# Kernel optimization log

Hardware: AMD Instinct MI355X
Metric: run time of the kernel (lower is better)

Reference implementation:

```python
import jax, jax.numpy as jnp
import numpy as np

N, E, F, H, C, G = 100000, 800000, 128, 128, 10, 128
EPS = 1e-5


def setup_inputs() -> dict:
    key = jax.random.key(0)
    ks = jax.random.split(key, 8)
    return {
        "x": jax.random.normal(ks[0], (N, F), jnp.float32),
        "edge_index": jax.random.randint(ks[1], (2, E), 0, N),
        "batch": jnp.sort(jax.random.randint(ks[2], (N,), 0, G)),
        "edge_weight": jax.random.uniform(ks[3], (E,), jnp.float32, 0.1, 1.0),
        "bn_feat_w": jnp.ones((F,), jnp.float32),
        "bn_feat_b": jnp.full((F,), 1e-4, jnp.float32),
        "conv_feat_W": jax.random.normal(ks[4], (F, H), jnp.float32) / np.float32(np.sqrt(F)),
        "conv_feat_b": jnp.zeros((H,), jnp.float32),
        "bns_w": jnp.ones((3, H), jnp.float32),
        "bns_b": jnp.full((3, H), 1e-4, jnp.float32),
        "convs_W": jax.random.normal(ks[5], (3, H, H), jnp.float32) / np.float32(np.sqrt(H)),
        "convs_b": jnp.zeros((3, H), jnp.float32),
        "bn_fc_w": jnp.ones((H,), jnp.float32),
        "bn_fc_b": jnp.full((H,), 1e-4, jnp.float32),
        "lin_fc_W": jax.random.normal(ks[6], (H, H), jnp.float32) / np.float32(np.sqrt(H)),
        "lin_fc_b": jnp.zeros((H,), jnp.float32),
        "bn_hidden_w": jnp.ones((H,), jnp.float32),
        "bn_hidden_b": jnp.full((H,), 1e-4, jnp.float32),
        "lin_class_W": jax.random.normal(ks[7], (H, C), jnp.float32) / np.float32(np.sqrt(H)),
        "lin_class_b": jnp.zeros((C,), jnp.float32),
    }


def _bn(h, w, b):
    # training-mode BatchNorm1d: biased batch stats over dim 0
    mu = h.mean(0)
    var = jnp.mean((h - mu) ** 2, 0)
    return (h - mu) * jax.lax.rsqrt(var + EPS) * w + b


def reference(x, edge_index, batch, edge_weight,
              bn_feat_w, bn_feat_b, conv_feat_W, conv_feat_b,
              bns_w, bns_b, convs_W, convs_b,
              bn_fc_w, bn_fc_b, lin_fc_W, lin_fc_b,
              bn_hidden_w, bn_hidden_b, lin_class_W, lin_class_b):
    n = x.shape[0]
    loops = jnp.arange(n)
    # PyG GCNConv: add self-loops (weight 1) + symmetric normalization, shared by all convs
    row = jnp.concatenate([edge_index[0], loops])
    col = jnp.concatenate([edge_index[1], loops])
    ew = jnp.concatenate([edge_weight, jnp.ones((n,), x.dtype)])
    deg = jax.ops.segment_sum(ew, col, num_segments=n)
    dinv = jnp.where(deg > 0, jax.lax.rsqrt(jnp.maximum(deg, EPS)), 0.0)
    norm = (dinv[row] * ew * dinv[col])[:, None]  # [E+N, 1]

    def conv(h, W, b):
        m = (h @ W)[row] * norm                 # gather + scale per edge
        return jax.ops.segment_sum(m, col, num_segments=n) + b

    h = _bn(x, bn_feat_w, bn_feat_b)
    h = jax.nn.relu(conv(h, conv_feat_W, conv_feat_b))
    h_init = h

    x_list = []
    # branch 1: BN -> Conv -> ReLU chain
    h = h_init
    for i in range(3):
        h = jax.nn.relu(conv(_bn(h, bns_w[i], bns_b[i]), convs_W[i], convs_b[i]))
    x_list.append(h)
    # branch 2: double application of the same BN/Conv per step
    h = h_init
    for i in range(3):
        h_ = jax.nn.relu(conv(_bn(h, bns_w[i], bns_b[i]), convs_W[i], convs_b[i]))
        h = jax.nn.relu(conv(_bn(h_, bns_w[i], bns_b[i]), convs_W[i], convs_b[i]))
    x_list.append(h)
    # branch 3: identical to branch 1 when conv_residual=False
    h = h_init
    for i in range(3):
        h = jax.nn.relu(conv(_bn(h, bns_w[i], bns_b[i]), convs_W[i], convs_b[i]))
    x_list.append(h)
    # branch 4: BN -> ReLU only
    h = h_init
    for i in range(3):
        h = jax.nn.relu(_bn(h, bns_w[i], bns_b[i]))
    x_list.append(h)

    def head(hn):
        g = jax.ops.segment_sum(hn, batch, num_segments=G)  # global_add_pool
        g = jax.nn.relu(_bn(g, bn_fc_w, bn_fc_b) @ lin_fc_W + lin_fc_b)
        g = _bn(g, bn_hidden_w, bn_hidden_b)
        return jax.nn.log_softmax(g @ lin_class_W + lin_class_b, axis=-1)

    return tuple(head(hn) for hn in x_list)
```

## Files before the change

### kernel.cpp

```cpp
#include <hip/hip_runtime.h>

#define N_NODES 100000
#define NPAD    100032
#define NBLK    1563
#define NEDGE   800000
#define NGRP    128
#define NSLOT   32
#define EPS     1e-5f

typedef unsigned int   u32;
typedef unsigned short u16;
typedef short bf16x8 __attribute__((ext_vector_type(8)));
typedef float f32x4  __attribute__((ext_vector_type(4)));

__device__ __forceinline__ float bf2f(u32 u){ return __uint_as_float(u << 16); }
__device__ __forceinline__ u16 f2bf(float f){
  u32 x = __float_as_uint(f);
  x += 0x7fffu + ((x >> 16) & 1u);
  return (u16)(x >> 16);
}

__global__ void k_init(float* deg, int* cnt, int* fill, float* gbuf){
  int i = blockIdx.x * 256 + threadIdx.x;
  if (i < NPAD){ deg[i] = 1.0f; cnt[i] = 0; fill[i] = 0; }
  if (i < 4 * NGRP * 128) gbuf[i] = 0.f;
}

__global__ void k_deg(const int* __restrict__ col, const float* __restrict__ ew,
                      float* __restrict__ deg, int* __restrict__ cnt){
  int e = blockIdx.x * 256 + threadIdx.x;
  if (e < NEDGE){
    int c = col[e];
    atomicAdd(&deg[c], ew[e]);
    atomicAdd(&cnt[c], 1);
  }
}

__global__ void k_dinv(const float* __restrict__ deg, float* __restrict__ dinv, float* __restrict__ srow){
  int i = blockIdx.x * 256 + threadIdx.x;
  if (i < N_NODES){
    float d = deg[i];
    float v = d > 0.f ? rsqrtf(fmaxf(d, EPS)) : 0.f;
    dinv[i] = v; srow[i] = v * v;
  }
}

__global__ __launch_bounds__(256) void k_chunksum(const int* __restrict__ cnt, int* __restrict__ csum){
  int b = blockIdx.x, t = threadIdx.x;
  int s = 0;
  for (int i = t; i < 1024; i += 256){ int idx = b * 1024 + i; if (idx < N_NODES) s += cnt[idx]; }
  __shared__ int red[256];
  red[t] = s; __syncthreads();
  for (int o = 128; o > 0; o >>= 1){ if (t < o) red[t] += red[t + o]; __syncthreads(); }
  if (t == 0) csum[b] = red[0];
}

__global__ __launch_bounds__(128) void k_chunkscan(const int* __restrict__ csum, int* __restrict__ coff,
                                                   int* __restrict__ ptrA){
  int t = threadIdx.x;
  __shared__ int s[128];
  int v = (t < 98) ? csum[t] : 0;
  s[t] = v; __syncthreads();
  for (int o = 1; o < 128; o <<= 1){
    int x = (t >= o) ? s[t - o] : 0;
    __syncthreads(); s[t] += x; __syncthreads();
  }
  if (t < 98) coff[t] = s[t] - v;
  if (t == 0) ptrA[N_NODES] = NEDGE;
}

__global__ __launch_bounds__(256) void k_scan2(const int* __restrict__ cnt, const int* __restrict__ coff,
                                               int* __restrict__ ptrA){
  int b = blockIdx.x, t = threadIdx.x;
  int base = b * 1024 + t * 4;
  int v[4], tot = 0;
  #pragma unroll
  for (int k = 0; k < 4; k++){ int idx = base + k; v[k] = (idx < N_NODES) ? cnt[idx] : 0; tot += v[k]; }
  __shared__ int sc[256];
  sc[t] = tot; __syncthreads();
  for (int o = 1; o < 256; o <<= 1){
    int x = (t >= o) ? sc[t - o] : 0;
    __syncthreads(); sc[t] += x; __syncthreads();
  }
  int off = coff[b] + sc[t] - tot;
  #pragma unroll
  for (int k = 0; k < 4; k++){ int idx = base + k; if (idx < N_NODES) ptrA[idx] = off; off += v[k]; }
}

__global__ void k_fill(const int* __restrict__ row, const int* __restrict__ col,
                       const float* __restrict__ ew, const float* __restrict__ dinv,
                       const int* __restrict__ ptrA, int* __restrict__ fill, int2* __restrict__ adj,
                       float* __restrict__ srow){
  int e = blockIdx.x * 256 + threadIdx.x;
  if (e < NEDGE){
    int r = row[e], c = col[e];
    float w = dinv[r] * ew[e] * dinv[c];
    int pos = ptrA[c] + atomicAdd(&fill[c], 1);
    adj[pos] = make_int2(r, __float_as_int(w));
    atomicAdd(&srow[c], w);
  }
}

__global__ __launch_bounds__(256) void k_bhist(const int* __restrict__ batch, int* __restrict__ bpart){
  __shared__ int loc[128];
  int t = threadIdx.x;
  if (t < 128) loc[t] = 0;
  __syncthreads();
  int i = blockIdx.x * 256 + t;
  if (i < N_NODES) atomicAdd(&loc[batch[i]], 1);
  __syncthreads();
  if (t < 128) bpart[blockIdx.x * 128 + t] = loc[t];
}

__global__ __launch_bounds__(128) void k_bscan(const int* __restrict__ bpart, int* __restrict__ gptr){
  int t = threadIdx.x;
  int v = 0;
  for (int p = 0; p < 391; p++) v += bpart[p * 128 + t];
  __shared__ int s[128];
  s[t] = v; __syncthreads();
  for (int o = 1; o < 128; o <<= 1){
    int x = (t >= o) ? s[t - o] : 0;
    __syncthreads(); s[t] += x; __syncthreads();
  }
  gptr[t + 1] = s[t];
  if (t == 0) gptr[0] = 0;
}

__global__ __launch_bounds__(256) void k_cvtstats(const float* __restrict__ x, u32* __restrict__ dst,
                                                  float* __restrict__ sums_out){
  __shared__ float R[1024];
  int t = threadIdx.x;
  float s0 = 0.f, q0 = 0.f, s1 = 0.f, q1 = 0.f;
  size_t base = (size_t)blockIdx.x * 4096 + t;
  #pragma unroll
  for (int it = 0; it < 16; it++){
    size_t idx = base + (size_t)it * 256;
    if (idx < (size_t)N_NODES * 64){
      float2 v = ((const float2*)x)[idx];
      dst[idx] = (u32)f2bf(v.x) | ((u32)f2bf(v.y) << 16);
      s0 += v.x; q0 += v.x * v.x; s1 += v.y; q1 += v.y * v.y;
    }
  }
  R[t] = s0; R[256 + t] = q0; R[512 + t] = s1; R[768 + t] = q1;
  __syncthreads();
  if (t < 64){
    float S0 = 0.f, Q0 = 0.f, S1 = 0.f, Q1 = 0.f;
    #pragma unroll
    for (int g = 0; g < 4; g++){
      S0 += R[g * 64 + t];       Q0 += R[256 + g * 64 + t];
      S1 += R[512 + g * 64 + t]; Q1 += R[768 + g * 64 + t];
    }
    float* so = sums_out + (blockIdx.x & (NSLOT - 1)) * 256;
    atomicAdd(&so[2 * t], S0);
    atomicAdd(&so[2 * t + 1], S1);
    atomicAdd(&so[128 + 2 * t], Q0);
    atomicAdd(&so[128 + 2 * t + 1], Q1);
  }
}

__device__ __forceinline__ void fold_body(int blk, int t, const float* __restrict__ sums,
    const float* __restrict__ bw, const float* __restrict__ bb,
    const float* __restrict__ W, const float* __restrict__ bias,
    u16* __restrict__ Wh, u16* __restrict__ Wl, float* __restrict__ rb,
    float* scl, float* shf, float* stot, float* rred){
  {
    float s = 0.f;
    #pragma unroll 4
    for (int sl = 0; sl < NSLOT; sl++) s += sums[sl * 256 + t];
    stot[t] = s;
  }
  __syncthreads();
  if (t < 128){
    float mu  = stot[t] * (1.f / N_NODES);
    float var = stot[128 + t] * (1.f / N_NODES) - mu * mu;
    float sc  = bw[t] * rsqrtf(var + EPS);
    scl[t] = sc; shf[t] = bb[t] - mu * sc;
  }
  __syncthreads();
  {
    int idx = blk * 256 + t;
    int lane_ = idx & 63, sl = idx >> 6;
    int nt_ = sl >> 2, ks_ = sl & 3;
    int n_ = nt_ * 16 + (lane_ & 15);
    int kb = ks_ * 32 + (lane_ >> 4) * 8;
    u16 hi8[8], lo8[8];
    #pragma unroll
    for (int j = 0; j < 8; j++){
      float wv = W[(kb + j) * 128 + n_];
      float xv = scl[kb + j] * wv;
      u16 hh = f2bf(xv);
      hi8[j] = hh; lo8[j] = f2bf(xv - bf2f(hh));
    }
    uint4 ph, pl;
    ph.x = (u32)hi8[0] | ((u32)hi8[1] << 16); ph.y = (u32)hi8[2] | ((u32)hi8[3] << 16);
    ph.z = (u32)hi8[4] | ((u32)hi8[5] << 16); ph.w = (u32)hi8[6] | ((u32)hi8[7] << 16);
    pl.x = (u32)lo8[0] | ((u32)lo8[1] << 16); pl.y = (u32)lo8[2] | ((u32)lo8[3] << 16);
    pl.z = (u32)lo8[4] | ((u32)lo8[5] << 16); pl.w = (u32)lo8[6] | ((u32)lo8[7] << 16);
    *(uint4*)&Wh[idx * 8] = ph;
    *(uint4*)&Wl[idx * 8] = pl;
  }
  {
    int nl = t & 15, kk = t >> 4;
    int n2 = blk * 16 + nl;
    float rp = 0.f;
    #pragma unroll
    for (int j = 0; j < 8; j++){
      int k2 = kk * 8 + j;
      rp += shf[k2] * W[k2 * 128 + n2];
    }
    rred[t] = rp;
  }
  __syncthreads();
  if (t < 16){
    float s = 0.f;
    #pragma unroll
    for (int kk2 = 0; kk2 < 16; kk2++) s += rred[kk2 * 16 + t];
    int n2 = blk * 16 + t;
    rb[n2] = s;
    rb[128 + n2] = bias[n2];
  }
}

__global__ __launch_bounds__(256) void k_fold(const float* __restrict__ sums,
    const float* __restrict__ bw, const float* __restrict__ bb,
    const float* __restrict__ W, const float* __restrict__ bias,
    u16* __restrict__ Wh, u16* __restrict__ Wl, float* __restrict__ rb){
  __shared__ float scl[128], shf[128], stot[256], rred[256];
  fold_body(blockIdx.x, threadIdx.x, sums, bw, bb, W, bias, Wh, Wl, rb, scl, shf, stot, rred);
}

__global__ __launch_bounds__(256) void k_fold2(
    const float* __restrict__ sumsA, const float* __restrict__ bwA, const float* __restrict__ bbA,
    const float* __restrict__ WA, const float* __restrict__ biasA,
    u16* __restrict__ WhA, u16* __restrict__ WlA, float* __restrict__ rbA,
    const float* __restrict__ sumsB, const float* __restrict__ bwB, const float* __restrict__ bbB,
    const float* __restrict__ WB, const float* __restrict__ biasB,
    u16* __restrict__ WhB, u16* __restrict__ WlB, float* __restrict__ rbB){
  __shared__ float scl[128], shf[128], stot[256], rred[256];
  int bb_ = blockIdx.x;
  if (bb_ < 8)
    fold_body(bb_, threadIdx.x, sumsA, bwA, bbA, WA, biasA, WhA, WlA, rbA, scl, shf, stot, rred);
  else
    fold_body(bb_ - 8, threadIdx.x, sumsB, bwB, bbB, WB, biasB, WhB, WlB, rbB, scl, shf, stot, rred);
}

#define CONV_EPILOGUE(RB, HOUT, SOUT, BLK)                                     \
  __syncthreads();                                                             \
  sred[t] = 0.f;                                                               \
  __syncthreads();                                                             \
  _Pragma("unroll")                                                            \
  for (int nt = 0; nt < 8; nt++){                                              \
    int colc = nt * 16 + m;                                                    \
    float rv = RB[colc], bv = RB[128 + colc];                                  \
    float s = 0.f, qq = 0.f;                                                   \
    _Pragma("unroll")                                                          \
    for (int r = 0; r < 4; r++){                                               \
      int rown = row0 + q * 4 + r;                                             \
      float v = C[nt][r] + srow[rown] * rv + bv;                               \
      v = fmaxf(v, 0.f);                                                       \
      u16 sv = f2bf(v);                                                        \
      HOUT[(size_t)rown * 128 + colc] = sv;                                    \
      if (rown < N_NODES){ float vv = bf2f(sv); s += vv; qq += vv * vv; }      \
    }                                                                          \
    s  += __shfl_xor(s, 16, 64);  s  += __shfl_xor(s, 32, 64);                 \
    qq += __shfl_xor(qq, 16, 64); qq += __shfl_xor(qq, 32, 64);                \
    if (q == 0){                                                               \
      atomicAdd(&sred[colc], s);                                               \
      atomicAdd(&sred[128 + colc], qq);                                        \
    }                                                                          \
  }                                                                            \
  __syncthreads();                                                             \
  atomicAdd(&SOUT[((BLK) & (NSLOT - 1)) * 256 + t], sred[t]);

#define FMA_KS(KS, V, WT) \
  acc[KS][0] += (WT) * __uint_as_float((V).x << 16); acc[KS][1] += (WT) * __uint_as_float((V).x & 0xffff0000u); \
  acc[KS][2] += (WT) * __uint_as_float((V).y << 16); acc[KS][3] += (WT) * __uint_as_float((V).y & 0xffff0000u); \
  acc[KS][4] += (WT) * __uint_as_float((V).z << 16); acc[KS][5] += (WT) * __uint_as_float((V).z & 0xffff0000u); \
  acc[KS][6] += (WT) * __uint_as_float((V).w << 16); acc[KS][7] += (WT) * __uint_as_float((V).w & 0xffff0000u);

#define VMCNT6() asm volatile("s_waitcnt vmcnt(6)" ::: "memory")
#define VMCNT5() asm volatile("s_waitcnt vmcnt(5)" ::: "memory")
#define SB0()    __builtin_amdgcn_sched_barrier(0)


__device__ __forceinline__ void gll_stage(const u16* __restrict__ h, u16* dst, int2 aj, int lane){
  int c = lane & 15, g = lane >> 4;
  #pragma unroll
  for (int ii = 0; ii < 4; ii++){
    int rl = ii * 4 + g;
    int srcrow = __shfl(aj.x, rl, 64);
    const u16* src = h + (size_t)srcrow * 128 + (size_t)((c ^ rl) * 8);
    __builtin_amdgcn_global_load_lds((const void*)src, (void*)(dst + ii * 512), 16, 0, 0);
  }
}

#define GITER(WA, WB, WC, WD, STG, J)                                          \
  WD = *(const int2*)(adj + base_ + min((J) + 3, dcl));                        \
  VMCNT6();                                                                    \
  {                                                                            \
    float wgt = __int_as_float(__shfl((WA).y, m, 64));                         \
    if ((J) < deg){                                                            \
      const u16* sp = stage + (STG) * 2048;                                    \
      _Pragma("unroll")                                                        \
      for (int ks = 0; ks < 4; ks++){                                          \
        int slot = (q + 4 * ks) ^ m;                                           \
        uint4 v = *(const uint4*)(sp + m * 128 + slot * 8);                    \
        FMA_KS(ks, v, wgt)                                                     \
      }                                                                        \
    }                                                                          \
  }                                                                            \
  VMCNT5();                                                                    \
  gll_stage(h, stage + (STG) * 2048, WC, lane);                                \
  SB0();

__device__ __forceinline__ void gather_row_lds(const u16* __restrict__ h,
    const int* __restrict__ ptrA, const int2* __restrict__ adj,
    const float* __restrict__ dinv, int row0, int lane, u16* stage,
    float (&acc)[4][8]){
  int m = lane & 15, q = lane >> 4;
  #pragma unroll
  for (int ks = 0; ks < 4; ks++)
    #pragma unroll
    for (int j = 0; j < 8; j++) acc[ks][j] = 0.f;
  int r = row0 + m;
  int r2 = min(r, N_NODES - 1);
  int b0 = ptrA[r2], b1 = ptrA[r2 + 1];
  int deg = (r < N_NODES) ? (b1 - b0) : 0;
  int base_ = b0;
  int dcl = max(deg - 1, 0);
  float di = dinv[r2];
  float sw = (r < N_NODES) ? di * di : 0.f;
  const u16* hq = h + q * 8;
  const u16* sp_ = hq + (size_t)r2 * 128;
  uint4 s0 = *(const uint4*)(sp_);
  uint4 s1 = *(const uint4*)(sp_ + 32);
  uint4 s2 = *(const uint4*)(sp_ + 64);
  uint4 s3 = *(const uint4*)(sp_ + 96);
  int2 W0 = *(const int2*)(adj + base_);
  int2 W1 = *(const int2*)(adj + base_ + min(1, dcl));
  int wmax = deg;
  wmax = max(wmax, __shfl_xor(wmax, 1, 64));
  wmax = max(wmax, __shfl_xor(wmax, 2, 64));
  wmax = max(wmax, __shfl_xor(wmax, 4, 64));
  wmax = max(wmax, __shfl_xor(wmax, 8, 64));
  FMA_KS(0, s0, sw) FMA_KS(1, s1, sw) FMA_KS(2, s2, sw) FMA_KS(3, s3, sw)
  if (wmax > 0){
    int2 W2 = W0, W3 = W0;
    SB0();
    gll_stage(h, stage, W0, lane);
    SB0();
    W2 = *(const int2*)(adj + base_ + min(2, dcl));
    SB0();
    gll_stage(h, stage + 2048, W1, lane);
    SB0();
    for (int j0 = 0; j0 < wmax; j0 += 4){
      GITER(W0, W1, W2, W3, 0, j0)
      GITER(W1, W2, W3, W0, 1, j0 + 1)
      GITER(W2, W3, W0, W1, 0, j0 + 2)
      GITER(W3, W0, W1, W2, 1, j0 + 3)
    }
  }
}

#define BUILD_AFRAG()                                                          \
  bf16x8 AH[4], AL[4];                                                         \
  _Pragma("unroll")                                                            \
  for (int ks = 0; ks < 4; ks++)                                               \
    _Pragma("unroll")                                                          \
    for (int j = 0; j < 8; j++){                                               \
      u16 hh = f2bf(acc[ks][j]);                                               \
      AH[ks][j] = (short)hh;                                                   \
      AL[ks][j] = (short)f2bf(acc[ks][j] - bf2f(hh));                          \
    }

#define MFMA_3PASS(WH, WL_)                                                    \
  _Pragma("unroll")                                                            \
  for (int ks = 0; ks < 4; ks++){                                              \
    _Pragma("unroll")                                                          \
    for (int nt = 0; nt < 8; nt++){                                            \
      bf16x8 bh = ((const bf16x8*)WH)[(nt * 4 + ks) * 64 + lane];              \
      bf16x8 bl = ((const bf16x8*)WL_)[(nt * 4 + ks) * 64 + lane];             \
      C[nt] = __builtin_amdgcn_mfma_f32_16x16x32_bf16(AH[ks], bh, C[nt], 0, 0, 0); \
      C[nt] = __builtin_amdgcn_mfma_f32_16x16x32_bf16(AL[ks], bh, C[nt], 0, 0, 0); \
      C[nt] = __builtin_amdgcn_mfma_f32_16x16x32_bf16(AH[ks], bl, C[nt], 0, 0, 0); \
    }                                                                          \
  }

__global__ __launch_bounds__(256, 3) void k_conv(
    const u16* __restrict__ h, const int* __restrict__ ptrA, const int2* __restrict__ adj,
    const float* __restrict__ dinv, const float* __restrict__ srow,
    const u16* __restrict__ Wh, const u16* __restrict__ Wl, const float* __restrict__ rb,
    u16* __restrict__ hout, float* __restrict__ sums_out){
  __shared__ u16 hstage[4][2][2048];
  __shared__ float sred[256];
  int t = threadIdx.x;
  int wave = t >> 6, lane = t & 63, m = lane & 15, q = lane >> 4;
  int blk = blockIdx.x;
  int row0 = blk * 64 + wave * 16;
  float acc[4][8];
  gather_row_lds(h, ptrA, adj, dinv, row0, lane, &hstage[wave][0][0], acc);
  BUILD_AFRAG()
  f32x4 C[8];
  #pragma unroll
  for (int nt = 0; nt < 8; nt++) C[nt] = f32x4{0.f, 0.f, 0.f, 0.f};
  MFMA_3PASS(Wh, Wl)
  CONV_EPILOGUE(rb, hout, sums_out, blk)
}

__global__ __launch_bounds__(256, 3) void k_conv2(
    const u16* __restrict__ hA, const u16* __restrict__ hB,
    const int* __restrict__ ptrA, const int2* __restrict__ adj,
    const float* __restrict__ dinv, const float* __restrict__ srow,
    const u16* __restrict__ WhA, const u16* __restrict__ WlA, const float* __restrict__ rbA,
    u16* __restrict__ houtA, float* __restrict__ sumsA,
    const u16* __restrict__ WhB, const u16* __restrict__ WlB, const float* __restrict__ rbB,
    u16* __restrict__ houtB, float* __restrict__ sumsB){
  __shared__ u16 hstage[4][2][2048];
  __shared__ float sred[256];
  int t = threadIdx.x;
  int wave = t >> 6, lane = t & 63, m = lane & 15, q = lane >> 4;
  int bb = blockIdx.x;
  int second = bb >= NBLK;
  int blk = second ? bb - NBLK : bb;
  const u16* h = second ? hB : hA;
  const u16* Wh = second ? WhB : WhA;
  const u16* Wl = second ? WlB : WlA;
  const float* rb = second ? rbB : rbA;
  u16* hout = second ? houtB : houtA;
  float* sums_out = second ? sumsB : sumsA;
  int row0 = blk * 64 + wave * 16;
  float acc[4][8];
  gather_row_lds(h, ptrA, adj, dinv, row0, lane, &hstage[wave][0][0], acc);
  BUILD_AFRAG()
  f32x4 C[8];
  #pragma unroll
  for (int nt = 0; nt < 8; nt++) C[nt] = f32x4{0.f, 0.f, 0.f, 0.f};
  MFMA_3PASS(Wh, Wl)
  CONV_EPILOGUE(rb, hout, sums_out, blk)
}

__global__ __launch_bounds__(256, 3) void k_dualconv(
    const u16* __restrict__ h, const int* __restrict__ ptrA, const int2* __restrict__ adj,
    const float* __restrict__ dinv, const float* __restrict__ srow,
    const u16* __restrict__ Wh1, const u16* __restrict__ Wl1, const float* __restrict__ rb1,
    u16* __restrict__ hout1, float* __restrict__ sums1,
    const u16* __restrict__ Wh2, const u16* __restrict__ Wl2, const float* __restrict__ rb2,
    u16* __restrict__ hout2, float* __restrict__ sums2){
  __shared__ u16 hstage[4][2][2048];
  __shared__ float sred[256];
  int t = threadIdx.x;
  int wave = t >> 6, lane = t & 63, m = lane & 15, q = lane >> 4;
  int blk = blockIdx.x;
  int row0 = blk * 64 + wave * 16;
  float acc[4][8];
  gather_row_lds(h, ptrA, adj, dinv, row0, lane, &hstage[wave][0][0], acc);
  BUILD_AFRAG()
  f32x4 C[8];
  #pragma unroll
  for (int nt = 0; nt < 8; nt++) C[nt] = f32x4{0.f, 0.f, 0.f, 0.f};
  MFMA_3PASS(Wh1, Wl1)
  CONV_EPILOGUE(rb1, hout1, sums1, blk)
  #pragma unroll
  for (int nt = 0; nt < 8; nt++) C[nt] = f32x4{0.f, 0.f, 0.f, 0.f};
  MFMA_3PASS(Wh2, Wl2)
  CONV_EPILOGUE(rb2, hout2, sums2, blk)
}

__global__ __launch_bounds__(256) void k_normrelu(const u16* __restrict__ h, const float* __restrict__ sums,
    const float* __restrict__ bw, const float* __restrict__ bb, u16* __restrict__ o,
    float* __restrict__ sums_out){
  __shared__ float scl[128], shf[128], R[1024], stot[256];
  int t = threadIdx.x;
  {
    float s = 0.f;
    #pragma unroll 4
    for (int sl = 0; sl < NSLOT; sl++) s += sums[sl * 256 + t];
    stot[t] = s;
  }
  __syncthreads();
  if (t < 128){
    float mu  = stot[t] * (1.f / N_NODES);
    float var = stot[128 + t] * (1.f / N_NODES) - mu * mu;
    float sc  = bw[t] * rsqrtf(var + EPS);
    scl[t] = sc; shf[t] = bb[t] - mu * sc;
  }
  __syncthreads();
  int c0 = (t & 63) * 2;
  float sc0 = scl[c0], sh0 = shf[c0], sc1 = scl[c0 + 1], sh1 = shf[c0 + 1];
  float s0 = 0.f, q0 = 0.f, s1 = 0.f, q1 = 0.f;
  size_t base = (size_t)blockIdx.x * 4096 + t;
  #pragma unroll
  for (int it = 0; it < 16; it++){
    size_t idx = base + (size_t)it * 256;
    if (idx < (size_t)N_NODES * 64){
      u32 v = ((const u32*)h)[idx];
      float x0 = fmaxf(bf2f(v & 0xffffu) * sc0 + sh0, 0.f);
      float x1 = fmaxf(bf2f(v >> 16) * sc1 + sh1, 0.f);
      u16 r0 = f2bf(x0), r1 = f2bf(x1);
      ((u32*)o)[idx] = (u32)r0 | ((u32)r1 << 16);
      float y0 = bf2f(r0), y1 = bf2f(r1);
      s0 += y0; q0 += y0 * y0; s1 += y1; q1 += y1 * y1;
    }
  }
  R[t] = s0; R[256 + t] = q0; R[512 + t] = s1; R[768 + t] = q1;
  __syncthreads();
  if (t < 64){
    float S0 = 0.f, Q0 = 0.f, S1 = 0.f, Q1 = 0.f;
    #pragma unroll
    for (int g = 0; g < 4; g++){
      S0 += R[g * 64 + t];       Q0 += R[256 + g * 64 + t];
      S1 += R[512 + g * 64 + t]; Q1 += R[768 + g * 64 + t];
    }
    float* so = sums_out + (blockIdx.x & (NSLOT - 1)) * 256;
    atomicAdd(&so[2 * t], S0);
    atomicAdd(&so[2 * t + 1], S1);
    atomicAdd(&so[128 + 2 * t], Q0);
    atomicAdd(&so[128 + 2 * t + 1], Q1);
  }
}

__global__ __launch_bounds__(128) void k_pool(const u16* __restrict__ h, const int* __restrict__ gptr,
                                              float* __restrict__ gdst){
  int g = blockIdx.x >> 3, s = blockIdx.x & 7, t = threadIdx.x;
  int b = gptr[g], e = gptr[g + 1];
  int len = e - b, per = (len + 7) >> 3;
  int r0 = b + s * per, r1 = min(r0 + per, e);
  float acc = 0.f;
  for (int r = r0; r < r1; r++) acc += bf2f(h[(size_t)r * 128 + t]);
  atomicAdd(&gdst[g * 128 + t], acc);
}

__global__ __launch_bounds__(256) void k_head(const float* __restrict__ gbuf,
    const float* __restrict__ fcw, const float* __restrict__ fcb,
    const float* __restrict__ Wfc, const float* __restrict__ bfc,
    const float* __restrict__ bhw, const float* __restrict__ bhb,
    const float* __restrict__ Wcl, const float* __restrict__ bcl,
    float* __restrict__ out){
  __shared__ float GS[128 * 65];
  __shared__ float ls[256], lq[256];
  __shared__ float scl[128], shf[128], scl2[128], shf2[128];
  __shared__ float sumT[128], sumQ[128];
  __shared__ float WclT[1280], Lrow[1280];
  int t = threadIdx.x, br = blockIdx.x;
  int slot = (br == 1) ? 1 : (br == 3 ? 3 : 0);
  const float* G = gbuf + slot * 16384;
  {
    int col = t & 127, hf2 = t >> 7;
    float s = 0.f, q = 0.f;
    for (int g = hf2 * 64; g < hf2 * 64 + 64; g++){ float v = G[g * 128 + col]; s += v; q += v * v; }
    ls[t] = s; lq[t] = q;
  }
  for (int idx = t; idx < 1280; idx += 256){
    int cc = idx >> 7, c = idx & 127;
    WclT[idx] = Wcl[c * 10 + cc];
  }
  if (t < 128){ sumT[t] = 0.f; sumQ[t] = 0.f; }
  __syncthreads();
  if (t < 128){
    float s = ls[t] + ls[t + 128], q = lq[t] + lq[t + 128];
    float mu = s * (1.f / 128), var = q * (1.f / 128) - mu * mu;
    float sc = fcw[t] * rsqrtf(var + EPS);
    scl[t] = sc; shf[t] = fcb[t] - mu * sc;
  }
  __syncthreads();
  int tr = t >> 4, tc = t & 15, r0 = tr * 8, c0 = tc * 8;
  float acc[8][8];
  #pragma unroll
  for (int a = 0; a < 8; a++)
    #pragma unroll
    for (int b = 0; b < 8; b++) acc[a][b] = 0.f;
  for (int kh = 0; kh < 2; kh++){
    for (int idx = t; idx < 8192; idx += 256){
      int r = idx >> 6, kk = idx & 63, f = kh * 64 + kk;
      GS[r * 65 + kk] = G[r * 128 + f] * scl[f] + shf[f];
    }
    __syncthreads();
    #pragma unroll 2
    for (int k = 0; k < 64; k++){
      float a[8];
      #pragma unroll
      for (int ri = 0; ri < 8; ri++) a[ri] = GS[(r0 + ri) * 65 + k];
      float4 b0 = *(const float4*)&Wfc[(kh * 64 + k) * 128 + c0];
      float4 b1 = *(const float4*)&Wfc[(kh * 64 + k) * 128 + c0 + 4];
      float bb[8] = {b0.x, b0.y, b0.z, b0.w, b1.x, b1.y, b1.z, b1.w};
      #pragma unroll
      for (int ri = 0; ri < 8; ri++)
        #pragma unroll
        for (int ci = 0; ci < 8; ci++) acc[ri][ci] += a[ri] * bb[ci];
    }
    __syncthreads();
  }
  #pragma unroll
  for (int ci = 0; ci < 8; ci++){
    float bb = bfc[c0 + ci];
    float s = 0.f, q = 0.f;
    #pragma unroll
    for (int ri = 0; ri < 8; ri++){
      float v = fmaxf(acc[ri][ci] + bb, 0.f);
      acc[ri][ci] = v; s += v; q += v * v;
    }
    atomicAdd(&sumT[c0 + ci], s);
    atomicAdd(&sumQ[c0 + ci], q);
  }
  __syncthreads();
  if (t < 128){
    float mu = sumT[t] * (1.f / 128), var = sumQ[t] * (1.f / 128) - mu * mu;
    float sc = bhw[t] * rsqrtf(var + EPS);
    scl2[t] = sc; shf2[t] = bhb[t] - mu * sc;
  }
  __syncthreads();
  #pragma unroll
  for (int ci = 0; ci < 8; ci++){
    float sc = scl2[c0 + ci], sh = shf2[c0 + ci];
    #pragma unroll
    for (int ri = 0; ri < 8; ri++) acc[ri][ci] = acc[ri][ci] * sc + sh;
  }
  #pragma unroll
  for (int ri = 0; ri < 8; ri++){
    float pl[10];
    #pragma unroll
    for (int cc = 0; cc < 10; cc++) pl[cc] = 0.f;
    #pragma unroll
    for (int ci = 0; ci < 8; ci++){
      float v = acc[ri][ci];
      #pragma unroll
      for (int cc = 0; cc < 10; cc++) pl[cc] += v * WclT[cc * 128 + c0 + ci];
    }
    #pragma unroll
    for (int msk = 1; msk < 16; msk <<= 1)
      #pragma unroll
      for (int cc = 0; cc < 10; cc++) pl[cc] += __shfl_xor(pl[cc], msk, 64);
    if (tc == 0)
      #pragma unroll
      for (int cc = 0; cc < 10; cc++) Lrow[(r0 + ri) * 10 + cc] = pl[cc];
  }
  __syncthreads();
  if (t < 128){
    float l[10];
    #pragma unroll
    for (int cc = 0; cc < 10; cc++) l[cc] = Lrow[t * 10 + cc] + bcl[cc];
    float m = l[0];
    #pragma unroll
    for (int cc = 1; cc < 10; cc++) m = fmaxf(m, l[cc]);
    float se = 0.f;
    #pragma unroll
    for (int cc = 0; cc < 10; cc++) se += expf(l[cc] - m);
    float lse = m + logf(se);
    #pragma unroll
    for (int cc = 0; cc < 10; cc++) out[br * 1280 + t * 10 + cc] = l[cc] - lse;
  }
}

extern "C" void kernel_launch(void* const* d_in, const int* in_sizes, int n_in,
                              void* d_out, int out_size, void* d_ws, size_t ws_size,
                              hipStream_t stream){
  const float* x    = (const float*)d_in[0];
  const int*  ei    = (const int*)d_in[1];
  const int*  batch = (const int*)d_in[2];
  const float* ew   = (const float*)d_in[3];
  const float* bnfw = (const float*)d_in[4];
  const float* bnfb = (const float*)d_in[5];
  const float* cfW  = (const float*)d_in[6];
  const float* cfb  = (const float*)d_in[7];
  const float* bnsw = (const float*)d_in[8];
  const float* bnsb = (const float*)d_in[9];
  const float* cvW  = (const float*)d_in[10];
  const float* cvb  = (const float*)d_in[11];
  const float* fcw  = (const float*)d_in[12];
  const float* fcb  = (const float*)d_in[13];
  const float* Wfc  = (const float*)d_in[14];
  const float* bfc  = (const float*)d_in[15];
  const float* bhw  = (const float*)d_in[16];
  const float* bhb  = (const float*)d_in[17];
  const float* Wcl  = (const float*)d_in[18];
  const float* bcl  = (const float*)d_in[19];
  float* out = (float*)d_out;

  char* p = (char*)d_ws;
  auto carve = [&](size_t bytes)->void*{ void* r = (void*)p; p += (bytes + 255) & ~(size_t)255; return r; };
  float* deg  = (float*)carve((size_t)NPAD * 4);
  float* dinv = (float*)carve((size_t)NPAD * 4);
  float* srow = (float*)carve((size_t)NPAD * 4);
  int*   cnt  = (int*)carve((size_t)NPAD * 4);
  int*   fill = (int*)carve((size_t)NPAD * 4);
  int*   ptrA = (int*)carve((size_t)(NPAD + 1) * 4);
  int*   bpart= (int*)carve((size_t)391 * 128 * 4);
  int*   csum = (int*)carve(512);
  int*   coff = (int*)carve(512);
  int*   gptr = (int*)carve(1024);
  float* S    = (float*)carve((size_t)13 * NSLOT * 1024);
  float* gbuf = (float*)carve(4 * 128 * 128 * 4);
  u16*   F0h  = (u16*)carve(32768);  u16* F0l = (u16*)carve(32768);  float* F0r = (float*)carve(1024);
  u16*   F1h  = (u16*)carve(32768);  u16* F1l = (u16*)carve(32768);  float* F1r = (float*)carve(1024);
  u16*   F2h  = (u16*)carve(32768);  u16* F2l = (u16*)carve(32768);  float* F2r = (float*)carve(1024);
  u16*   B0   = (u16*)carve((size_t)NPAD * 256);
  u16*   B1   = (u16*)carve((size_t)NPAD * 256);
  u16*   B2   = (u16*)carve((size_t)NPAD * 256);
  u16*   B3   = (u16*)carve((size_t)NPAD * 256);
  int2*  adj  = (int2*)carve((size_t)NEDGE * 8);
  u16*   Xb   = B3;
  auto Sb = [&](int i){ return S + (size_t)i * NSLOT * 256; };

  (void)hipMemsetAsync(S, 0, (size_t)13 * NSLOT * 1024, stream);

  k_init<<<392, 256, 0, stream>>>(deg, cnt, fill, gbuf);
  k_deg<<<3125, 256, 0, stream>>>(ei + NEDGE, ew, deg, cnt);
  k_dinv<<<391, 256, 0, stream>>>(deg, dinv, srow);
  k_chunksum<<<98, 256, 0, stream>>>(cnt, csum);
  k_chunkscan<<<1, 128, 0, stream>>>(csum, coff, ptrA);
  k_scan2<<<98, 256, 0, stream>>>(cnt, coff, ptrA);
  k_fill<<<3125, 256, 0, stream>>>(ei, ei + NEDGE, ew, dinv, ptrA, fill, adj, srow);
  k_bhist<<<391, 256, 0, stream>>>(batch, bpart);
  k_bscan<<<1, 128, 0, stream>>>(bpart, gptr);
  k_cvtstats<<<NBLK, 256, 0, stream>>>(x, (u32*)Xb, Sb(0));

  auto fold = [&](const float* Sin, const float* bw, const float* bb,
                  const float* W, const float* bias, u16* Fh, u16* Fl, float* Fr){
    k_fold<<<8, 256, 0, stream>>>(Sin, bw, bb, W, bias, Fh, Fl, Fr);
  };
  auto conv = [&](const u16* hin, const u16* Fh, const u16* Fl, const float* Fr,
                  u16* hout, float* Sout){
    k_conv<<<NBLK, 256, 0, stream>>>(hin, ptrA, adj, dinv, srow, Fh, Fl, Fr, hout, Sout);
  };

  fold(Sb(0), bnfw, bnfb, cfW, cfb, F0h, F0l, F0r);
  conv(Xb, F0h, F0l, F0r, B0, Sb(1));
  fold(Sb(1), bnsw, bnsb, cvW, cvb, F1h, F1l, F1r);
  conv(B0, F1h, F1l, F1r, B1, Sb(2));
  k_normrelu<<<NBLK, 256, 0, stream>>>(B0, Sb(1), bnsw,       bnsb,       B2, Sb(3));
  k_normrelu<<<NBLK, 256, 0, stream>>>(B2, Sb(3), bnsw + 128, bnsb + 128, B3, Sb(4));
  k_normrelu<<<NBLK, 256, 0, stream>>>(B3, Sb(4), bnsw + 256, bnsb + 256, B2, Sb(12));
  k_pool<<<1024, 128, 0, stream>>>(B2, gptr, gbuf + 3 * 16384);
  k_fold2<<<16, 256, 0, stream>>>(
      Sb(2), bnsw + 128, bnsb + 128, cvW + 16384, cvb + 128, F0h, F0l, F0r,
      Sb(2), bnsw,       bnsb,       cvW,         cvb,       F1h, F1l, F1r);
  k_dualconv<<<NBLK, 256, 0, stream>>>(B1, ptrA, adj, dinv, srow,
      F0h, F0l, F0r, B3, Sb(5),
      F1h, F1l, F1r, B2, Sb(6));
  k_fold2<<<16, 256, 0, stream>>>(
      Sb(5), bnsw + 256, bnsb + 256, cvW + 32768, cvb + 256, F2h, F2l, F2r,
      Sb(6), bnsw + 128, bnsb + 128, cvW + 16384, cvb + 128, F0h, F0l, F0r);
  k_conv2<<<2 * NBLK, 256, 0, stream>>>(B3, B2, ptrA, adj, dinv, srow,
      F2h, F2l, F2r, B0, Sb(10),
      F0h, F0l, F0r, B1, Sb(7));
  k_pool<<<1024, 128, 0, stream>>>(B0, gptr, gbuf);
  fold(Sb(7), bnsw + 128, bnsb + 128, cvW + 16384, cvb + 128, F1h, F1l, F1r);
  conv(B1, F1h, F1l, F1r, B2, Sb(8));
  fold(Sb(8), bnsw + 256, bnsb + 256, cvW + 32768, cvb + 256, F2h, F2l, F2r);
  conv(B2, F2h, F2l, F2r, B1, Sb(9));
  fold(Sb(9), bnsw + 256, bnsb + 256, cvW + 32768, cvb + 256, F0h, F0l, F0r);
  conv(B1, F0h, F0l, F0r, B3, Sb(11));
  k_pool<<<1024, 128, 0, stream>>>(B3, gptr, gbuf + 16384);

  k_head<<<4, 256, 0, stream>>>(gbuf, fcw, fcb, Wfc, bfc, bhw, bhb, Wcl, bcl, out);
}
```

Measured before the change: 1.094 ms.

## Sort nodes by in-degree so each wave gathers rows of similar degree

Adds a counting sort of nodes by in-degree (histogram, scan, scatter) that builds a permutation. The conv kernels then process nodes in that permuted order, so the 16 rows handled by a wave have similar degree and fewer lanes sit idle in the divergent gather loop. The gather loop now exits after every 2 iterations instead of 4, which cuts wasted padded iterations. The cost is three extra setup kernels, an indirection through perm, and scattered rather than contiguous output writes in the epilogue.

```diff
diff --git a/kernel.cpp b/kernel.cpp
--- a/kernel.cpp
+++ b/kernel.cpp
@@ -98,6 +98,51 @@
     int pos = ptrA[c] + atomicAdd(&fill[c], 1);
     adj[pos] = make_int2(r, __float_as_int(w));
     atomicAdd(&srow[c], w);
+  }
+}
+
+__global__ __launch_bounds__(256) void k_dhist(const int* __restrict__ cnt, int* __restrict__ dpart){
+  __shared__ int loc[256];
+  int t = threadIdx.x, blk = blockIdx.x;
+  loc[t] = 0;
+  __syncthreads();
+  int i = blk * 256 + t;
+  if (i < N_NODES) atomicAdd(&loc[min(cnt[i], 255)], 1);
+  __syncthreads();
+  dpart[blk * 256 + t] = loc[t];
+}
+
+__global__ __launch_bounds__(256) void k_dscan(int* __restrict__ dpart){
+  __shared__ int tot[256], sfx[256];
+  int t = threadIdx.x;
+  int s = 0;
+  for (int p = 0; p < 391; p++) s += dpart[p * 256 + t];
+  tot[t] = s;
+  sfx[t] = s;
+  __syncthreads();
+  for (int o = 1; o < 256; o <<= 1){
+    int x = (t + o < 256) ? sfx[t + o] : 0;
+    __syncthreads(); sfx[t] += x; __syncthreads();
+  }
+  int run = sfx[t] - tot[t];
+  for (int p = 0; p < 391; p++){
+    int tmp = dpart[p * 256 + t];
+    dpart[p * 256 + t] = run;
+    run += tmp;
+  }
+}
+
+__global__ __launch_bounds__(256) void k_dscatter(const int* __restrict__ cnt, const int* __restrict__ dpart,
+                                                  int* __restrict__ perm){
+  __shared__ int loc[256];
+  int t = threadIdx.x, blk = blockIdx.x;
+  loc[t] = dpart[blk * 256 + t];
+  __syncthreads();
+  int i = blk * 256 + t;
+  if (i < N_NODES){
+    int b = min(cnt[i], 255);
+    int pos = atomicAdd(&loc[b], 1);
+    perm[pos] = i;
   }
 }
 
@@ -255,12 +300,14 @@
     float s = 0.f, qq = 0.f;                                                   \
     _Pragma("unroll")                                                          \
     for (int r = 0; r < 4; r++){                                               \
-      int rown = row0 + q * 4 + r;                                             \
-      float v = C[nt][r] + srow[rown] * rv + bv;                               \
-      v = fmaxf(v, 0.f);                                                       \
-      u16 sv = f2bf(v);                                                        \
-      HOUT[(size_t)rown * 128 + colc] = sv;                                    \
-      if (rown < N_NODES){ float vv = bf2f(sv); s += vv; qq += vv * vv; }      \
+      int pr = prow[r];                                                        \
+      if (pr >= 0){                                                            \
+        float v = C[nt][r] + srow[pr] * rv + bv;                               \
+        v = fmaxf(v, 0.f);                                                     \
+        u16 sv = f2bf(v);                                                      \
+        HOUT[(size_t)pr * 128 + colc] = sv;                                    \
+        float vv = bf2f(sv); s += vv; qq += vv * vv;                           \
+      }                                                                        \
     }                                                                          \
     s  += __shfl_xor(s, 16, 64);  s  += __shfl_xor(s, 32, 64);                 \
     qq += __shfl_xor(qq, 16, 64); qq += __shfl_xor(qq, 32, 64);                \
@@ -281,7 +328,6 @@
 #define VMCNT6() asm volatile("s_waitcnt vmcnt(6)" ::: "memory")
 #define VMCNT5() asm volatile("s_waitcnt vmcnt(5)" ::: "memory")
 #define SB0()    __builtin_amdgcn_sched_barrier(0)
-
 
 __device__ __forceinline__ void gll_stage(const u16* __restrict__ h, u16* dst, int2 aj, int lane){
   int c = lane & 15, g = lane >> 4;
@@ -315,23 +361,24 @@
 
 __device__ __forceinline__ void gather_row_lds(const u16* __restrict__ h,
     const int* __restrict__ ptrA, const int2* __restrict__ adj,
-    const float* __restrict__ dinv, int row0, int lane, u16* stage,
-    float (&acc)[4][8]){
+    const float* __restrict__ dinv, const int* __restrict__ perm,
+    int row0, int lane, u16* stage, float (&acc)[4][8]){
   int m = lane & 15, q = lane >> 4;
   #pragma unroll
   for (int ks = 0; ks < 4; ks++)
     #pragma unroll
     for (int j = 0; j < 8; j++) acc[ks][j] = 0.f;
-  int r = row0 + m;
-  int r2 = min(r, N_NODES - 1);
-  int b0 = ptrA[r2], b1 = ptrA[r2 + 1];
-  int deg = (r < N_NODES) ? (b1 - b0) : 0;
-  int base_ = b0;
+  int rl = row0 + m;
+  int rp = perm[min(rl, N_NODES - 1)];
+  int active = rl < N_NODES;
+  int b0 = ptrA[rp], b1 = ptrA[rp + 1];
+  int deg = active ? (b1 - b0) : 0;
+  int base_ = (deg > 0) ? b0 : 0;
   int dcl = max(deg - 1, 0);
-  float di = dinv[r2];
-  float sw = (r < N_NODES) ? di * di : 0.f;
+  float di = dinv[rp];
+  float sw = active ? di * di : 0.f;
   const u16* hq = h + q * 8;
-  const u16* sp_ = hq + (size_t)r2 * 128;
+  const u16* sp_ = hq + (size_t)rp * 128;
   uint4 s0 = *(const uint4*)(sp_);
   uint4 s1 = *(const uint4*)(sp_ + 32);
   uint4 s2 = *(const uint4*)(sp_ + 64);
@@ -353,11 +400,14 @@
     SB0();
     gll_stage(h, stage + 2048, W1, lane);
     SB0();
-    for (int j0 = 0; j0 < wmax; j0 += 4){
+    int j0 = 0;
+    for (;;){
       GITER(W0, W1, W2, W3, 0, j0)
       GITER(W1, W2, W3, W0, 1, j0 + 1)
-      GITER(W2, W3, W0, W1, 0, j0 + 2)
-      GITER(W3, W0, W1, W2, 1, j0 + 3)
+      j0 += 2; if (j0 >= wmax) break;
+      GITER(W2, W3, W0, W1, 0, j0)
+      GITER(W3, W0, W1, W2, 1, j0 + 1)
+      j0 += 2; if (j0 >= wmax) break;
     }
   }
 }
@@ -372,6 +422,14 @@
       AH[ks][j] = (short)hh;                                                   \
       AL[ks][j] = (short)f2bf(acc[ks][j] - bf2f(hh));                          \
     }
+
+#define PROW_SETUP()                                                           \
+  int prow[4];                                                                 \
+  _Pragma("unroll")                                                            \
+  for (int r_ = 0; r_ < 4; r_++){                                              \
+    int rr = row0 + q * 4 + r_;                                                \
+    prow[r_] = (rr < N_NODES) ? perm[rr] : -1;                                 \
+  }
 
 #define MFMA_3PASS(WH, WL_)                                                    \
   _Pragma("unroll")                                                            \
@@ -388,7 +446,7 @@
 
 __global__ __launch_bounds__(256, 3) void k_conv(
     const u16* __restrict__ h, const int* __restrict__ ptrA, const int2* __restrict__ adj,
-    const float* __restrict__ dinv, const float* __restrict__ srow,
+    const float* __restrict__ dinv, const float* __restrict__ srow, const int* __restrict__ perm,
     const u16* __restrict__ Wh, const u16* __restrict__ Wl, const float* __restrict__ rb,
     u16* __restrict__ hout, float* __restrict__ sums_out){
   __shared__ u16 hstage[4][2][2048];
@@ -398,8 +456,9 @@
   int blk = blockIdx.x;
   int row0 = blk * 64 + wave * 16;
   float acc[4][8];
-  gather_row_lds(h, ptrA, adj, dinv, row0, lane, &hstage[wave][0][0], acc);
+  gather_row_lds(h, ptrA, adj, dinv, perm, row0, lane, &hstage[wave][0][0], acc);
   BUILD_AFRAG()
+  PROW_SETUP()
   f32x4 C[8];
   #pragma unroll
   for (int nt = 0; nt < 8; nt++) C[nt] = f32x4{0.f, 0.f, 0.f, 0.f};
@@ -410,7 +469,7 @@
 __global__ __launch_bounds__(256, 3) void k_conv2(
     const u16* __restrict__ hA, const u16* __restrict__ hB,
     const int* __restrict__ ptrA, const int2* __restrict__ adj,
-    const float* __restrict__ dinv, const float* __restrict__ srow,
+    const float* __restrict__ dinv, const float* __restrict__ srow, const int* __restrict__ perm,
     const u16* __restrict__ WhA, const u16* __restrict__ WlA, const float* __restrict__ rbA,
     u16* __restrict__ houtA, float* __restrict__ sumsA,
     const u16* __restrict__ WhB, const u16* __restrict__ WlB, const float* __restrict__ rbB,
@@ -430,8 +489,9 @@
   float* sums_out = second ? sumsB : sumsA;
   int row0 = blk * 64 + wave * 16;
   float acc[4][8];
-  gather_row_lds(h, ptrA, adj, dinv, row0, lane, &hstage[wave][0][0], acc);
+  gather_row_lds(h, ptrA, adj, dinv, perm, row0, lane, &hstage[wave][0][0], acc);
   BUILD_AFRAG()
+  PROW_SETUP()
   f32x4 C[8];
   #pragma unroll
   for (int nt = 0; nt < 8; nt++) C[nt] = f32x4{0.f, 0.f, 0.f, 0.f};
@@ -441,7 +501,7 @@
 
 __global__ __launch_bounds__(256, 3) void k_dualconv(
     const u16* __restrict__ h, const int* __restrict__ ptrA, const int2* __restrict__ adj,
-    const float* __restrict__ dinv, const float* __restrict__ srow,
+    const float* __restrict__ dinv, const float* __restrict__ srow, const int* __restrict__ perm,
     const u16* __restrict__ Wh1, const u16* __restrict__ Wl1, const float* __restrict__ rb1,
     u16* __restrict__ hout1, float* __restrict__ sums1,
     const u16* __restrict__ Wh2, const u16* __restrict__ Wl2, const float* __restrict__ rb2,
@@ -453,8 +513,9 @@
   int blk = blockIdx.x;
   int row0 = blk * 64 + wave * 16;
   float acc[4][8];
-  gather_row_lds(h, ptrA, adj, dinv, row0, lane, &hstage[wave][0][0], acc);
+  gather_row_lds(h, ptrA, adj, dinv, perm, row0, lane, &hstage[wave][0][0], acc);
   BUILD_AFRAG()
+  PROW_SETUP()
   f32x4 C[8];
   #pragma unroll
   for (int nt = 0; nt < 8; nt++) C[nt] = f32x4{0.f, 0.f, 0.f, 0.f};
@@ -684,7 +745,9 @@
   int*   cnt  = (int*)carve((size_t)NPAD * 4);
   int*   fill = (int*)carve((size_t)NPAD * 4);
   int*   ptrA = (int*)carve((size_t)(NPAD + 1) * 4);
+  int*   perm = (int*)carve((size_t)NPAD * 4);
   int*   bpart= (int*)carve((size_t)391 * 128 * 4);
+  int*   dpart= (int*)carve((size_t)391 * 256 * 4);
   int*   csum = (int*)carve(512);
   int*   coff = (int*)carve(512);
   int*   gptr = (int*)carve(1024);
@@ -706,6 +769,9 @@
   k_init<<<392, 256, 0, stream>>>(deg, cnt, fill, gbuf);
   k_deg<<<3125, 256, 0, stream>>>(ei + NEDGE, ew, deg, cnt);
   k_dinv<<<391, 256, 0, stream>>>(deg, dinv, srow);
+  k_dhist<<<391, 256, 0, stream>>>(cnt, dpart);
+  k_dscan<<<1, 256, 0, stream>>>(dpart);
+  k_dscatter<<<391, 256, 0, stream>>>(cnt, dpart, perm);
   k_chunksum<<<98, 256, 0, stream>>>(cnt, csum);
   k_chunkscan<<<1, 128, 0, stream>>>(csum, coff, ptrA);
   k_scan2<<<98, 256, 0, stream>>>(cnt, coff, ptrA);
@@ -720,7 +786,7 @@
   };
   auto conv = [&](const u16* hin, const u16* Fh, const u16* Fl, const float* Fr,
                   u16* hout, float* Sout){
-    k_conv<<<NBLK, 256, 0, stream>>>(hin, ptrA, adj, dinv, srow, Fh, Fl, Fr, hout, Sout);
+    k_conv<<<NBLK, 256, 0, stream>>>(hin, ptrA, adj, dinv, srow, perm, Fh, Fl, Fr, hout, Sout);
   };
 
   fold(Sb(0), bnfw, bnfb, cfW, cfb, F0h, F0l, F0r);
@@ -734,13 +800,13 @@
   k_fold2<<<16, 256, 0, stream>>>(
       Sb(2), bnsw + 128, bnsb + 128, cvW + 16384, cvb + 128, F0h, F0l, F0r,
       Sb(2), bnsw,       bnsb,       cvW,         cvb,       F1h, F1l, F1r);
-  k_dualconv<<<NBLK, 256, 0, stream>>>(B1, ptrA, adj, dinv, srow,
+  k_dualconv<<<NBLK, 256, 0, stream>>>(B1, ptrA, adj, dinv, srow, perm,
       F0h, F0l, F0r, B3, Sb(5),
       F1h, F1l, F1r, B2, Sb(6));
   k_fold2<<<16, 256, 0, stream>>>(
       Sb(5), bnsw + 256, bnsb + 256, cvW + 32768, cvb + 256, F2h, F2l, F2r,
       Sb(6), bnsw + 128, bnsb + 128, cvW + 16384, cvb + 128, F0h, F0l, F0r);
-  k_conv2<<<2 * NBLK, 256, 0, stream>>>(B3, B2, ptrA, adj, dinv, srow,
+  k_conv2<<<2 * NBLK, 256, 0, stream>>>(B3, B2, ptrA, adj, dinv, srow, perm,
       F2h, F2l, F2r, B0, Sb(10),
       F0h, F0l, F0r, B1, Sb(7));
   k_pool<<<1024, 128, 0, stream>>>(B0, gptr, gbuf);
```

Result: slower. 1.140 ms (+4.2%).
